# Kernel optimization log

Measured on AMD Instinct MI355X. Metric: run time of the kernel, lower is better.

## Reference

```python
import jax, jax.numpy as jnp
import numpy as np

N_NODE = 4096
K = 32           # num_nearest_neighbors
HIDDEN = 128
RMS_EPS = 1e-5
DT = 0.01        # init scale for linear weights (init_linear_weights(..., scale=dt))


def _rmsnorm(x, g):
    # RMSNorm over last dim with learned scale (eqx.nn.RMSNorm-style)
    return x * jax.lax.rsqrt(jnp.mean(x * x, axis=-1, keepdims=True) + RMS_EPS) * g


def _pos_mlp(x, W1, b1, g1, W2, b2, g2, W3, b3):
    # MLPWithLayerNorm(in=2, width=HIDDEN, depth=2, out=1, act=silu, rms_norm=True):
    # per hidden layer: Linear -> RMSNorm -> SiLU; final Linear with identity activation.
    h = jax.nn.silu(_rmsnorm(x @ W1.T + b1, g1))
    h = jax.nn.silu(_rmsnorm(h @ W2.T + b2, g2))
    return h @ W3.T + b3  # [E, 1]


def setup_inputs() -> dict:
    key = jax.random.key(0)
    ks = jax.random.split(key, 8)

    def xavier(k, shape):
        fan_in, fan_out = shape[1], shape[0]
        std = jnp.sqrt(2.0 / (fan_in + fan_out))
        return (jax.random.normal(k, shape, dtype=jnp.float32) * std * DT)

    return {
        "pos": jax.random.normal(ks[0], (N_NODE, 3), dtype=jnp.float32),
        "t": jax.random.uniform(ks[1], (1,), dtype=jnp.float32),
        "W1": xavier(ks[2], (HIDDEN, 2)),
        "b1": jnp.zeros((HIDDEN,), dtype=jnp.float32),
        "g1": jnp.ones((HIDDEN,), dtype=jnp.float32),
        "W2": xavier(ks[3], (HIDDEN, HIDDEN)),
        "b2": jnp.zeros((HIDDEN,), dtype=jnp.float32),
        "g2": jnp.ones((HIDDEN,), dtype=jnp.float32),
        "W3": xavier(ks[4], (1, HIDDEN)),
        "b3": jnp.zeros((1,), dtype=jnp.float32),
    }


def reference(pos, t, W1, b1, g1, W2, b2, g2, W3, b3):
    n = pos.shape[0]
    # Pairwise squared distances for kNN graph build
    diff = pos[:, None, :] - pos[None, :, :]              # [n, n, 3]
    radial_full = jnp.sum(diff * diff, axis=-1)           # [n, n]
    masked = radial_full.at[jnp.diag_indices(n)].set(jnp.inf)
    _, recv = jax.lax.top_k(-masked, k=K)                 # [n, K] nearest neighbors
    senders = jnp.repeat(jnp.arange(n), K)                # [n*K]
    receivers = recv.reshape(-1)                          # [n*K]

    # Gather edge geometry (normalize=False)
    coord_diff = pos[senders] - pos[receivers]            # [E, 3]
    radial = jnp.sum(coord_diff * coord_diff, axis=1, keepdims=True)  # [E, 1]

    # Per-edge MLP on [radial, t]
    t_scalar = jnp.reshape(t, ())
    edge_features = jnp.concatenate(
        [radial, jnp.full_like(radial, t_scalar)], axis=-1)          # [E, 2]
    edge_scalars = _pos_mlp(edge_features, W1, b1, g1, W2, b2, g2, W3, b3).squeeze(-1)

    # Scatter-sum messages back to sender nodes, average by neighbor count
    trans = coord_diff * edge_scalars[:, None]            # [E, 3]
    seg_sum = jax.ops.segment_sum(trans, senders, num_segments=n)    # [n, 3]
    seg_count = jnp.maximum(float(K), 1.0)
    return pos + seg_sum / seg_count
```

## Files before the change

### kernel.cpp

```cpp
#include <hip/hip_runtime.h>
#include <stdint.h>

#define NN   4096
#define KK   32
#define HID  128
#define BLK  256
#define WPB  4
#define GRID (NN / WPB)
#define CAP  128

typedef unsigned short bf16_t;
typedef __attribute__((ext_vector_type(8))) short bf16x8;
typedef __attribute__((ext_vector_type(4))) float f32x4;

#define FINF __uint_as_float(0x7f800000u)

__device__ __forceinline__ uint32_t pk2bf(float lo, float hi) {
    uint32_t r;
    asm("v_cvt_pk_bf16_f32 %0, %1, %2" : "=v"(r) : "v"(lo), "v"(hi));
    return r;
}
__device__ __forceinline__ float fastrcp(float x) {
    float r; asm("v_rcp_f32 %0, %1" : "=v"(r) : "v"(x)); return r;
}
__device__ __forceinline__ float fastrsq(float x) {
    float r; asm("v_rsq_f32 %0, %1" : "=v"(r) : "v"(x)); return r;
}
__device__ __forceinline__ float siluf(float x) {
    return x * fastrcp(1.0f + __expf(-x));
}

__device__ __forceinline__ void dist4(const float4* __restrict__ p4, int g, int lane,
                                      float px, float py, float pz,
                                      float d[4]) {
    float4 f0 = p4[g*192 + 3*lane];
    float4 f1 = p4[g*192 + 3*lane + 1];
    float4 f2 = p4[g*192 + 3*lane + 2];
    float jx[4] = {f0.x, f0.w, f1.z, f2.y};
    float jy[4] = {f0.y, f1.x, f1.w, f2.z};
    float jz[4] = {f0.z, f1.y, f2.x, f2.w};
    #pragma unroll
    for (int c = 0; c < 4; ++c) {
        float dx = px - jx[c], dy = py - jy[c], dz = pz - jz[c];
        d[c] = __fadd_rn(__fadd_rn(__fmul_rn(dx,dx), __fmul_rn(dy,dy)),
                         __fmul_rn(dz,dz));
    }
}

__global__ __launch_bounds__(256) void prepack_w2(
    const float* __restrict__ W2, uint4* __restrict__ w2b)
{
    int c  = blockIdx.x * 256 + threadIdx.x;
    int f  = c >> 6, ln = c & 63;
    int NT = f >> 2, kk = f & 3;
    int row = NT*16 + (ln & 15);
    int k0  = kk*32 + (ln >> 4) * 8;
    const float* s = W2 + row * HID + k0;
    float4 lo = *(const float4*)s;
    float4 hi = *(const float4*)(s + 4);
    uint4 pk;
    pk.x = pk2bf(lo.x, lo.y);
    pk.y = pk2bf(lo.z, lo.w);
    pk.z = pk2bf(hi.x, hi.y);
    pk.w = pk2bf(hi.z, hi.w);
    w2b[c] = pk;
}

template<bool WS>
struct __align__(16) Sm {
    union __align__(16) U {
        ushort dbf[NN];
        ushort h1[KK * HID];
    } uw[WPB];
    uint32_t cand[WPB][CAP];
    float    rads[WPB][KK];
    float    sedge[WPB][KK];
    int      recvs[WPB][KK];
    uint32_t w2l[WS ? 4 : HID * 64];
};

template<bool WS>
__global__ __launch_bounds__(BLK) void egnn_main(
    const float* __restrict__ pos, const float* __restrict__ tptr,
    const float* __restrict__ W1,  const float* __restrict__ b1,
    const float* __restrict__ g1,  const float* __restrict__ W2,
    const float* __restrict__ b2,  const float* __restrict__ g2,
    const float* __restrict__ W3,  const float* __restrict__ b3,
    const uint4* __restrict__ w2b, float* __restrict__ out)
{
    __shared__ Sm<WS> sm;
    const int tid  = threadIdx.x;
    const int lane = tid & 63;
    const int wid  = tid >> 6;
    const int i    = blockIdx.x * WPB + wid;
    const int l15  = lane & 15, lq = lane >> 4;

    const float ts  = tptr[0];
    const float b3s = b3[0];

    float A2, AC, C2;
    {
        const float4 w1v = ((const float4*)W1)[lane];
        const float2 b1v = ((const float2*)b1)[lane];
        float t0 = ts * w1v.y + b1v.x;
        float t1 = ts * w1v.w + b1v.y;
        A2 = w1v.x*w1v.x + w1v.z*w1v.z;
        AC = w1v.x*t0    + w1v.z*t1;
        C2 = t0*t0       + t1*t1;
        #pragma unroll
        for (int m = 32; m >= 1; m >>= 1) {
            A2 += __shfl_xor(A2, m, 64);
            AC += __shfl_xor(AC, m, 64);
            C2 += __shfl_xor(C2, m, 64);
        }
    }

    if constexpr (!WS) {
        for (int idx = tid; idx < HID * 16; idx += BLK) {
            int row = idx >> 4, c = idx & 15;
            const float* src = W2 + row * HID + c * 8;
            float4 lo = *(const float4*)src;
            float4 hi = *(const float4*)(src + 4);
            uint4 pk;
            pk.x = pk2bf(lo.x, lo.y);
            pk.y = pk2bf(lo.z, lo.w);
            pk.z = pk2bf(hi.x, hi.y);
            pk.w = pk2bf(hi.z, hi.w);
            *((uint4*)&sm.w2l[row * 64 + 4 * (c ^ (row & 15))]) = pk;
        }
        __syncthreads();
    }

    const float px = pos[3*i], py = pos[3*i+1], pz = pos[3*i+2];
    const float4* p4 = (const float4*)pos;

    const int  sgrp     = i >> 8;
    const bool selfLane = ((i >> 2) & 63) == lane;
    const int  selfc    = i & 3;

    float mind = FINF;
    {
        ushort* dbf = sm.uw[wid].dbf;
        #pragma unroll 4
        for (int g = 0; g < 16; ++g) {
            float d[4];
            dist4(p4, g, lane, px, py, pz, d);
            if (g == sgrp && selfLane) {
                #pragma unroll
                for (int c = 0; c < 4; ++c)
                    if (c == selfc) d[c] = FINF;
            }
            uint32_t lo = (__float_as_uint(d[0]) >> 16) | (__float_as_uint(d[1]) & 0xffff0000u);
            uint32_t hi = (__float_as_uint(d[2]) >> 16) | (__float_as_uint(d[3]) & 0xffff0000u);
            *((uint2*)&dbf[g*256 + 4*lane]) = make_uint2(lo, hi);
            mind = fminf(fminf(fminf(mind, d[0]), fminf(d[1], d[2])), d[3]);
        }
    }
    const uint32_t m16 = __float_as_uint(mind) >> 16;

    uint32_t v = 0;
    #pragma unroll
    for (int b = 15; b >= 0; --b) {
        uint32_t t = v | (1u << b);
        int nl = (int)__popcll(__ballot(m16 < t));
        if (nl < KK) v = t;
    }

    uint32_t cnt = 0;
    {
        const ushort* dbf = sm.uw[wid].dbf;
        uint32_t myc = 0;
        #pragma unroll 4
        for (int g = 0; g < 16; ++g) {
            uint2 w = *((const uint2*)&dbf[g*256 + 4*lane]);
            myc += (uint32_t)((w.x & 0xffffu) <= v);
            myc += (uint32_t)((w.x >> 16)     <= v);
            myc += (uint32_t)((w.y & 0xffffu) <= v);
            myc += (uint32_t)((w.y >> 16)     <= v);
        }
        uint32_t inc = myc;
        #pragma unroll
        for (int off = 1; off < 64; off <<= 1) {
            uint32_t y = __shfl_up(inc, off, 64);
            if (lane >= off) inc += y;
        }
        uint32_t slot = inc - myc;
        cnt = (uint32_t)__shfl((int)inc, 63, 64);
        if (myc) {
            #pragma unroll 4
            for (int g = 0; g < 16; ++g) {
                uint2 w = *((const uint2*)&dbf[g*256 + 4*lane]);
                uint32_t d16v[4] = {w.x & 0xffffu, w.x >> 16, w.y & 0xffffu, w.y >> 16};
                #pragma unroll
                for (int c = 0; c < 4; ++c) {
                    if (d16v[c] <= v) {
                        if (slot < CAP)
                            sm.cand[wid][slot] = (d16v[c] << 16)
                                               | (unsigned)(g*256 + 4*lane + c);
                        slot++;
                    }
                }
            }
        }
    }
    const int cntv = (int)cnt;

    if (cntv <= CAP) {
        for (int idx = cntv + lane; idx < CAP; idx += 64)
            sm.cand[wid][idx] = 0xffffffffu;

        #pragma unroll
        for (int h = 0; h < 2; ++h) {
            int idx = h*64 + lane;
            if (idx < cntv) {
                uint32_t km = sm.cand[wid][idx];
                int rank = 0;
                #pragma unroll 4
                for (int q = 0; q < CAP; q += 16) {
                    const uint4* cp = (const uint4*)&sm.cand[wid][q];
                    uint4 u0 = cp[0];
                    uint4 u1 = cp[1];
                    uint4 u2 = cp[2];
                    uint4 u3 = cp[3];
                    rank += (u0.x < km) ? 1 : 0;
                    rank += (u0.y < km) ? 1 : 0;
                    rank += (u0.z < km) ? 1 : 0;
                    rank += (u0.w < km) ? 1 : 0;
                    rank += (u1.x < km) ? 1 : 0;
                    rank += (u1.y < km) ? 1 : 0;
                    rank += (u1.z < km) ? 1 : 0;
                    rank += (u1.w < km) ? 1 : 0;
                    rank += (u2.x < km) ? 1 : 0;
                    rank += (u2.y < km) ? 1 : 0;
                    rank += (u2.z < km) ? 1 : 0;
                    rank += (u2.w < km) ? 1 : 0;
                    rank += (u3.x < km) ? 1 : 0;
                    rank += (u3.y < km) ? 1 : 0;
                    rank += (u3.z < km) ? 1 : 0;
                    rank += (u3.w < km) ? 1 : 0;
                }
                if (rank < KK) sm.recvs[wid][rank] = (int)(km & 0xFFFFu);
            }
        }
    } else {
        unsigned long long locmask = 0ull;
        if (selfLane)
            locmask |= 1ull << ((sgrp << 2) | selfc);
        for (int it = 0; it < KK; ++it) {
            unsigned long long best = ~0ull;
            for (int g = 0; g < 16; ++g) {
                float d[4];
                dist4(p4, g, lane, px, py, pz, d);
                #pragma unroll
                for (int c = 0; c < 4; ++c) {
                    bool dead = ((locmask >> (g*4 + c)) & 1ull) != 0ull;
                    unsigned long long key = dead ? ~0ull
                        : ((((unsigned long long)__float_as_uint(d[c])) << 12)
                           | (unsigned)(g*256 + 4*lane + c));
                    best = best < key ? best : key;
                }
            }
            #pragma unroll
            for (int m = 32; m >= 1; m >>= 1) {
                unsigned long long o = __shfl_xor(best, m, 64);
                best = best < o ? best : o;
            }
            int j = (int)(best & 0xfffull);
            if (lane == 0) sm.recvs[wid][it] = j;
            if (((j >> 2) & 63) == lane)
                locmask |= 1ull << ((j >> 8) * 4 + (j & 3));
        }
    }

    float cdx = 0.f, cdy = 0.f, cdz = 0.f;
    if (lane < KK) {
        int r = sm.recvs[wid][lane];
        cdx = px - pos[3*r];
        cdy = py - pos[3*r+1];
        cdz = pz - pos[3*r+2];
        float rad = __fadd_rn(__fadd_rn(__fmul_rn(cdx,cdx), __fmul_rn(cdy,cdy)),
                              __fmul_rn(cdz,cdz));
        sm.rads[wid][lane] = rad;
    }

    {
        const int ch = lane >> 2, epr = lane & 3;
        float4 wA = ((const float4*)W1)[ch*4    ];
        float4 wB = ((const float4*)W1)[ch*4 + 1];
        float4 wC = ((const float4*)W1)[ch*4 + 2];
        float4 wD = ((const float4*)W1)[ch*4 + 3];
        float4 bA = ((const float4*)b1)[ch*2], bB = ((const float4*)b1)[ch*2 + 1];
        float4 gA = ((const float4*)g1)[ch*2], gB = ((const float4*)g1)[ch*2 + 1];
        float av[8] = {wA.x, wA.z, wB.x, wB.z, wC.x, wC.z, wD.x, wD.z};
        float cv[8] = {ts*wA.y + bA.x, ts*wA.w + bA.y, ts*wB.y + bA.z, ts*wB.w + bA.w,
                       ts*wC.y + bB.x, ts*wC.w + bB.y, ts*wD.y + bB.z, ts*wD.w + bB.w};
        float gv[8] = {gA.x, gA.y, gA.z, gA.w, gB.x, gB.y, gB.z, gB.w};
        uint4* h1q = (uint4*)&sm.uw[wid].h1[0];
        #pragma unroll
        for (int g = 0; g < 8; ++g) {
            int E = 4*g + epr;
            float rad = sm.rads[wid][E];
            float sqv = rad*rad*A2 + 2.0f*rad*AC + C2;
            float rn  = fastrsq(sqv * (1.0f/HID) + 1e-5f);
            uint32_t pk[4];
            #pragma unroll
            for (int p = 0; p < 4; ++p) {
                float va = siluf((rad*av[2*p]   + cv[2*p])   * rn * gv[2*p]);
                float vb = siluf((rad*av[2*p+1] + cv[2*p+1]) * rn * gv[2*p+1]);
                pk[p] = pk2bf(va, vb);
            }
            h1q[E*16 + (ch ^ (E & 15))] = uint4{pk[0], pk[1], pk[2], pk[3]};
        }
    }

    float g2v[8], w3v[8], b2v[8];
    #pragma unroll
    for (int nt = 0; nt < 8; ++nt) {
        int n = nt*16 + l15;
        g2v[nt] = g2[n]; w3v[nt] = W3[n]; b2v[nt] = b2[n];
    }

    const bf16x8* h1v = (const bf16x8*)&sm.uw[wid].h1[0];
    #pragma unroll
    for (int mt = 0; mt < 2; ++mt) {
        f32x4 acc[8];
        #pragma unroll
        for (int nt = 0; nt < 8; ++nt) acc[nt] = f32x4{0.f, 0.f, 0.f, 0.f};
        const int m = mt*16 + l15;
        if constexpr (WS) {
            const bf16x8* bv = (const bf16x8*)w2b;
            #pragma unroll
            for (int kk = 0; kk < 4; ++kk) {
                bf16x8 af = h1v[m*16 + ((kk*4 + lq) ^ l15)];
                #pragma unroll
                for (int nt = 0; nt < 8; ++nt)
                    acc[nt] = __builtin_amdgcn_mfma_f32_16x16x32_bf16(
                                  af, bv[(nt*4 + kk)*64 + lane], acc[nt], 0, 0, 0);
            }
        } else {
            const bf16x8* w2v = (const bf16x8*)sm.w2l;
            #pragma unroll
            for (int kk = 0; kk < 4; ++kk) {
                const int q = (kk*4 + lq) ^ l15;
                bf16x8 af = h1v[m*16 + q];
                #pragma unroll
                for (int nt = 0; nt < 8; ++nt)
                    acc[nt] = __builtin_amdgcn_mfma_f32_16x16x32_bf16(
                                  af, w2v[(nt*16 + l15)*16 + q], acc[nt], 0, 0, 0);
            }
        }

        float ss[4];
        #pragma unroll
        for (int r = 0; r < 4; ++r) {
            float t = 0.f;
            #pragma unroll
            for (int nt = 0; nt < 8; ++nt) {
                float zz = acc[nt][r] + b2v[nt];
                acc[nt][r] = zz;
                t += zz*zz;
            }
            ss[r] = t;
        }
        #pragma unroll
        for (int m2 = 1; m2 <= 8; m2 <<= 1) {
            #pragma unroll
            for (int r = 0; r < 4; ++r) ss[r] += __shfl_xor(ss[r], m2, 64);
        }
        float sp[4];
        #pragma unroll
        for (int r = 0; r < 4; ++r) {
            float rn = fastrsq(ss[r] * (1.0f/HID) + 1e-5f);
            float t = 0.f;
            #pragma unroll
            for (int nt = 0; nt < 8; ++nt)
                t += siluf(acc[nt][r] * rn * g2v[nt]) * w3v[nt];
            sp[r] = t;
        }
        #pragma unroll
        for (int m2 = 1; m2 <= 8; m2 <<= 1) {
            #pragma unroll
            for (int r = 0; r < 4; ++r) sp[r] += __shfl_xor(sp[r], m2, 64);
        }
        if (l15 == 0) {
            #pragma unroll
            for (int r = 0; r < 4; ++r)
                sm.sedge[wid][mt*16 + lq*4 + r] = sp[r] + b3s;
        }
    }

    float mx = 0.f, my = 0.f, mz = 0.f;
    if (lane < KK) {
        float s = sm.sedge[wid][lane];
        mx = cdx * s; my = cdy * s; mz = cdz * s;
    }
    #pragma unroll
    for (int m = 32; m >= 1; m >>= 1) {
        mx += __shfl_xor(mx, m, 64);
        my += __shfl_xor(my, m, 64);
        mz += __shfl_xor(mz, m, 64);
    }
    if (lane == 0) {
        out[3*i    ] = px + mx * (1.0f/KK);
        out[3*i + 1] = py + my * (1.0f/KK);
        out[3*i + 2] = pz + mz * (1.0f/KK);
    }
}

extern "C" void kernel_launch(void* const* d_in, const int* in_sizes, int n_in,
                              void* d_out, int out_size, void* d_ws, size_t ws_size,
                              hipStream_t stream) {
    (void)in_sizes; (void)n_in; (void)out_size;
    const float* pos = (const float*)d_in[0];
    const float* t   = (const float*)d_in[1];
    const float* W1  = (const float*)d_in[2];
    const float* b1  = (const float*)d_in[3];
    const float* g1  = (const float*)d_in[4];
    const float* W2  = (const float*)d_in[5];
    const float* b2  = (const float*)d_in[6];
    const float* g2  = (const float*)d_in[7];
    const float* W3  = (const float*)d_in[8];
    const float* b3  = (const float*)d_in[9];
    float* out = (float*)d_out;

    if (d_ws != nullptr && ws_size >= 32768) {
        prepack_w2<<<8, 256, 0, stream>>>(W2, (uint4*)d_ws);
        egnn_main<true><<<GRID, BLK, 0, stream>>>(
            pos, t, W1, b1, g1, W2, b2, g2, W3, b3, (const uint4*)d_ws, out);
    } else {
        egnn_main<false><<<GRID, BLK, 0, stream>>>(
            pos, t, W1, b1, g1, W2, b2, g2, W3, b3, nullptr, out);
    }
}
```

Before: 109.3 us.

## Vectorize kNN distance math and register-buffer candidates to skip rescan

```diff
diff --git a/kernel.cpp b/kernel.cpp
--- a/kernel.cpp
+++ b/kernel.cpp
@@ -12,6 +12,7 @@
 typedef unsigned short bf16_t;
 typedef __attribute__((ext_vector_type(8))) short bf16x8;
 typedef __attribute__((ext_vector_type(4))) float f32x4;
+typedef __attribute__((ext_vector_type(2))) float f32x2;
 
 #define FINF __uint_as_float(0x7f800000u)
 
@@ -30,21 +31,29 @@
     return x * fastrcp(1.0f + __expf(-x));
 }
 
-__device__ __forceinline__ void dist4(const float4* __restrict__ p4, int g, int lane,
-                                      float px, float py, float pz,
-                                      float d[4]) {
+__device__ __forceinline__ void dist4v(const float4* __restrict__ p4, int g, int lane,
+                                       f32x2 pxv, f32x2 pyv, f32x2 pzv,
+                                       f32x2& d01, f32x2& d23) {
     float4 f0 = p4[g*192 + 3*lane];
     float4 f1 = p4[g*192 + 3*lane + 1];
     float4 f2 = p4[g*192 + 3*lane + 2];
-    float jx[4] = {f0.x, f0.w, f1.z, f2.y};
-    float jy[4] = {f0.y, f1.x, f1.w, f2.z};
-    float jz[4] = {f0.z, f1.y, f2.x, f2.w};
-    #pragma unroll
-    for (int c = 0; c < 4; ++c) {
-        float dx = px - jx[c], dy = py - jy[c], dz = pz - jz[c];
-        d[c] = __fadd_rn(__fadd_rn(__fmul_rn(dx,dx), __fmul_rn(dy,dy)),
-                         __fmul_rn(dz,dz));
-    }
+    f32x2 jx0 = {f0.x, f0.w}, jx1 = {f1.z, f2.y};
+    f32x2 jy0 = {f0.y, f1.x}, jy1 = {f1.w, f2.z};
+    f32x2 jz0 = {f0.z, f1.y}, jz1 = {f2.x, f2.w};
+    {
+#pragma clang fp contract(off)
+        f32x2 dx0 = pxv - jx0, dy0 = pyv - jy0, dz0 = pzv - jz0;
+        f32x2 dx1 = pxv - jx1, dy1 = pyv - jy1, dz1 = pzv - jz1;
+        d01 = dx0*dx0 + dy0*dy0 + dz0*dz0;
+        d23 = dx1*dx1 + dy1*dy1 + dz1*dz1;
+    }
+}
+__device__ __forceinline__ void dist4s(const float4* __restrict__ p4, int g, int lane,
+                                       float px, float py, float pz, float d[4]) {
+    f32x2 pxv = {px, px}, pyv = {py, py}, pzv = {pz, pz};
+    f32x2 a, b;
+    dist4v(p4, g, lane, pxv, pyv, pzv, a, b);
+    d[0] = a.x; d[1] = a.y; d[2] = b.x; d[3] = b.y;
 }
 
 __global__ __launch_bounds__(256) void prepack_w2(
@@ -133,6 +142,7 @@
 
     const float px = pos[3*i], py = pos[3*i+1], pz = pos[3*i+2];
     const float4* p4 = (const float4*)pos;
+    const f32x2 pxv = {px, px}, pyv = {py, py}, pzv = {pz, pz};
 
     const int  sgrp     = i >> 8;
     const bool selfLane = ((i >> 2) & 63) == lane;
@@ -143,17 +153,21 @@
         ushort* dbf = sm.uw[wid].dbf;
         #pragma unroll 4
         for (int g = 0; g < 16; ++g) {
-            float d[4];
-            dist4(p4, g, lane, px, py, pz, d);
+            f32x2 d01, d23;
+            dist4v(p4, g, lane, pxv, pyv, pzv, d01, d23);
             if (g == sgrp && selfLane) {
-                #pragma unroll
-                for (int c = 0; c < 4; ++c)
-                    if (c == selfc) d[c] = FINF;
-            }
-            uint32_t lo = (__float_as_uint(d[0]) >> 16) | (__float_as_uint(d[1]) & 0xffff0000u);
-            uint32_t hi = (__float_as_uint(d[2]) >> 16) | (__float_as_uint(d[3]) & 0xffff0000u);
+                d01.x = (selfc == 0) ? FINF : d01.x;
+                d01.y = (selfc == 1) ? FINF : d01.y;
+                d23.x = (selfc == 2) ? FINF : d23.x;
+                d23.y = (selfc == 3) ? FINF : d23.y;
+            }
+            uint2 u0 = *(uint2*)&d01;
+            uint2 u1 = *(uint2*)&d23;
+            uint32_t lo = (u0.x >> 16) | (u0.y & 0xffff0000u);
+            uint32_t hi = (u1.x >> 16) | (u1.y & 0xffff0000u);
             *((uint2*)&dbf[g*256 + 4*lane]) = make_uint2(lo, hi);
-            mind = fminf(fminf(fminf(mind, d[0]), fminf(d[1], d[2])), d[3]);
+            f32x2 mm = __builtin_elementwise_min(d01, d23);
+            mind = fminf(mind, fminf(mm.x, mm.y));
         }
     }
     const uint32_t m16 = __float_as_uint(mind) >> 16;
@@ -167,26 +181,46 @@
     }
 
     uint32_t cnt = 0;
+    uint32_t myc = 0;
     {
         const ushort* dbf = sm.uw[wid].dbf;
-        uint32_t myc = 0;
+        uint32_t s0 = 0, s1 = 0, s2 = 0, s3 = 0, s4 = 0, s5 = 0;
         #pragma unroll 4
         for (int g = 0; g < 16; ++g) {
             uint2 w = *((const uint2*)&dbf[g*256 + 4*lane]);
-            myc += (uint32_t)((w.x & 0xffffu) <= v);
-            myc += (uint32_t)((w.x >> 16)     <= v);
-            myc += (uint32_t)((w.y & 0xffffu) <= v);
-            myc += (uint32_t)((w.y >> 16)     <= v);
+            uint32_t e[4] = {w.x & 0xffffu, w.x >> 16, w.y & 0xffffu, w.y >> 16};
+            #pragma unroll
+            for (int c = 0; c < 4; ++c) {
+                if (e[c] <= v) {
+                    uint32_t key = (e[c] << 16) | (unsigned)(g*256 + 4*lane + c);
+                    s0 = (myc == 0) ? key : s0;
+                    s1 = (myc == 1) ? key : s1;
+                    s2 = (myc == 2) ? key : s2;
+                    s3 = (myc == 3) ? key : s3;
+                    s4 = (myc == 4) ? key : s4;
+                    s5 = (myc == 5) ? key : s5;
+                    myc++;
+                }
+            }
         }
         uint32_t inc = myc;
         #pragma unroll
         for (int off = 1; off < 64; off <<= 1) {
-            uint32_t y = __shfl_up(inc, off, 64);
+            uint32_t y = (uint32_t)__shfl_up((int)inc, off, 64);
             if (lane >= off) inc += y;
         }
         uint32_t slot = inc - myc;
         cnt = (uint32_t)__shfl((int)inc, 63, 64);
-        if (myc) {
+
+        const bool ovf = __ballot(myc > 6) != 0ull;
+        if (!ovf) {
+            if (myc > 0 && slot     < CAP) sm.cand[wid][slot    ] = s0;
+            if (myc > 1 && slot + 1 < CAP) sm.cand[wid][slot + 1] = s1;
+            if (myc > 2 && slot + 2 < CAP) sm.cand[wid][slot + 2] = s2;
+            if (myc > 3 && slot + 3 < CAP) sm.cand[wid][slot + 3] = s3;
+            if (myc > 4 && slot + 4 < CAP) sm.cand[wid][slot + 4] = s4;
+            if (myc > 5 && slot + 5 < CAP) sm.cand[wid][slot + 5] = s5;
+        } else if (myc) {
             #pragma unroll 4
             for (int g = 0; g < 16; ++g) {
                 uint2 w = *((const uint2*)&dbf[g*256 + 4*lane]);
@@ -209,15 +243,15 @@
         for (int idx = cntv + lane; idx < CAP; idx += 64)
             sm.cand[wid][idx] = 0xffffffffu;
 
+        const int nb = (cntv + 15) >> 4;
         #pragma unroll
         for (int h = 0; h < 2; ++h) {
             int idx = h*64 + lane;
             if (idx < cntv) {
                 uint32_t km = sm.cand[wid][idx];
                 int rank = 0;
-                #pragma unroll 4
-                for (int q = 0; q < CAP; q += 16) {
-                    const uint4* cp = (const uint4*)&sm.cand[wid][q];
+                for (int q = 0; q < nb; ++q) {
+                    const uint4* cp = (const uint4*)&sm.cand[wid][q*16];
                     uint4 u0 = cp[0];
                     uint4 u1 = cp[1];
                     uint4 u2 = cp[2];
@@ -250,7 +284,7 @@
             unsigned long long best = ~0ull;
             for (int g = 0; g < 16; ++g) {
                 float d[4];
-                dist4(p4, g, lane, px, py, pz, d);
+                dist4s(p4, g, lane, px, py, pz, d);
                 #pragma unroll
                 for (int c = 0; c < 4; ++c) {
                     bool dead = ((locmask >> (g*4 + c)) & 1ull) != 0ull;
```

New measurement: 108.0 us. No clear change (-1.2%).

## Pack distance math, use LDS atomics for candidate compaction, bound rank loop

Applied to the files above, without the earlier changes.

```diff
diff --git a/kernel.cpp b/kernel.cpp
--- a/kernel.cpp
+++ b/kernel.cpp
@@ -12,6 +12,7 @@
 typedef unsigned short bf16_t;
 typedef __attribute__((ext_vector_type(8))) short bf16x8;
 typedef __attribute__((ext_vector_type(4))) float f32x4;
+typedef __attribute__((ext_vector_type(2))) float f32x2;
 
 #define FINF __uint_as_float(0x7f800000u)
 
@@ -29,10 +30,15 @@
 __device__ __forceinline__ float siluf(float x) {
     return x * fastrcp(1.0f + __expf(-x));
 }
-
-__device__ __forceinline__ void dist4(const float4* __restrict__ p4, int g, int lane,
-                                      float px, float py, float pz,
-                                      float d[4]) {
+__device__ __forceinline__ f32x2 pk_add(f32x2 a, f32x2 b) {
+    f32x2 r; asm("v_pk_add_f32 %0, %1, %2" : "=v"(r) : "v"(a), "v"(b)); return r;
+}
+__device__ __forceinline__ f32x2 pk_sq(f32x2 a) {
+    f32x2 r; asm("v_pk_mul_f32 %0, %1, %1" : "=v"(r) : "v"(a)); return r;
+}
+
+__device__ __forceinline__ void dist4s(const float4* __restrict__ p4, int g, int lane,
+                                       float px, float py, float pz, float d[4]) {
     float4 f0 = p4[g*192 + 3*lane];
     float4 f1 = p4[g*192 + 3*lane + 1];
     float4 f2 = p4[g*192 + 3*lane + 2];
@@ -73,6 +79,7 @@
         ushort h1[KK * HID];
     } uw[WPB];
     uint32_t cand[WPB][CAP];
+    uint32_t ccnt[WPB];
     float    rads[WPB][KK];
     float    sedge[WPB][KK];
     int      recvs[WPB][KK];
@@ -95,6 +102,8 @@
     const int i    = blockIdx.x * WPB + wid;
     const int l15  = lane & 15, lq = lane >> 4;
 
+    if (lane == 0) sm.ccnt[wid] = 0;
+
     const float ts  = tptr[0];
     const float b3s = b3[0];
 
@@ -133,6 +142,7 @@
 
     const float px = pos[3*i], py = pos[3*i+1], pz = pos[3*i+2];
     const float4* p4 = (const float4*)pos;
+    const f32x2 nPxy = {-px, -py}, nPzx = {-pz, -px}, nPyz = {-py, -pz};
 
     const int  sgrp     = i >> 8;
     const bool selfLane = ((i >> 2) & 63) == lane;
@@ -143,17 +153,31 @@
         ushort* dbf = sm.uw[wid].dbf;
         #pragma unroll 4
         for (int g = 0; g < 16; ++g) {
-            float d[4];
-            dist4(p4, g, lane, px, py, pz, d);
+            float4 f0 = p4[g*192 + 3*lane];
+            float4 f1 = p4[g*192 + 3*lane+1];
+            float4 f2 = p4[g*192 + 3*lane+2];
+            f32x2 S0 = pk_sq(pk_add(f32x2{f0.x, f0.y}, nPxy));
+            f32x2 S1 = pk_sq(pk_add(f32x2{f0.z, f0.w}, nPzx));
+            f32x2 S2 = pk_sq(pk_add(f32x2{f1.x, f1.y}, nPyz));
+            f32x2 S3 = pk_sq(pk_add(f32x2{f1.z, f1.w}, nPxy));
+            f32x2 S4 = pk_sq(pk_add(f32x2{f2.x, f2.y}, nPzx));
+            f32x2 S5 = pk_sq(pk_add(f32x2{f2.z, f2.w}, nPyz));
+            float d0 = S0.x + S0.y + S1.x;
+            float d1 = S1.y + S2.x + S2.y;
+            float d2 = S3.x + S3.y + S4.x;
+            float d3 = S4.y + S5.x + S5.y;
             if (g == sgrp && selfLane) {
-                #pragma unroll
-                for (int c = 0; c < 4; ++c)
-                    if (c == selfc) d[c] = FINF;
-            }
-            uint32_t lo = (__float_as_uint(d[0]) >> 16) | (__float_as_uint(d[1]) & 0xffff0000u);
-            uint32_t hi = (__float_as_uint(d[2]) >> 16) | (__float_as_uint(d[3]) & 0xffff0000u);
+                d0 = (selfc == 0) ? FINF : d0;
+                d1 = (selfc == 1) ? FINF : d1;
+                d2 = (selfc == 2) ? FINF : d2;
+                d3 = (selfc == 3) ? FINF : d3;
+            }
+            uint32_t lo = __builtin_amdgcn_perm(__float_as_uint(d1),
+                                                __float_as_uint(d0), 0x07060302u);
+            uint32_t hi = __builtin_amdgcn_perm(__float_as_uint(d3),
+                                                __float_as_uint(d2), 0x07060302u);
             *((uint2*)&dbf[g*256 + 4*lane]) = make_uint2(lo, hi);
-            mind = fminf(fminf(fminf(mind, d[0]), fminf(d[1], d[2])), d[3]);
+            mind = fminf(fminf(fminf(mind, d0), fminf(d1, d2)), d3);
         }
     }
     const uint32_t m16 = __float_as_uint(mind) >> 16;
@@ -166,42 +190,29 @@
         if (nl < KK) v = t;
     }
 
-    uint32_t cnt = 0;
+    uint32_t cnt;
     {
         const ushort* dbf = sm.uw[wid].dbf;
-        uint32_t myc = 0;
+        const uint32_t vk  = (v << 16) | 0xffffu;
+        const uint32_t jb0 = 4*lane;
         #pragma unroll 4
         for (int g = 0; g < 16; ++g) {
             uint2 w = *((const uint2*)&dbf[g*256 + 4*lane]);
-            myc += (uint32_t)((w.x & 0xffffu) <= v);
-            myc += (uint32_t)((w.x >> 16)     <= v);
-            myc += (uint32_t)((w.y & 0xffffu) <= v);
-            myc += (uint32_t)((w.y >> 16)     <= v);
-        }
-        uint32_t inc = myc;
-        #pragma unroll
-        for (int off = 1; off < 64; off <<= 1) {
-            uint32_t y = __shfl_up(inc, off, 64);
-            if (lane >= off) inc += y;
-        }
-        uint32_t slot = inc - myc;
-        cnt = (uint32_t)__shfl((int)inc, 63, 64);
-        if (myc) {
-            #pragma unroll 4
-            for (int g = 0; g < 16; ++g) {
-                uint2 w = *((const uint2*)&dbf[g*256 + 4*lane]);
-                uint32_t d16v[4] = {w.x & 0xffffu, w.x >> 16, w.y & 0xffffu, w.y >> 16};
-                #pragma unroll
-                for (int c = 0; c < 4; ++c) {
-                    if (d16v[c] <= v) {
-                        if (slot < CAP)
-                            sm.cand[wid][slot] = (d16v[c] << 16)
-                                               | (unsigned)(g*256 + 4*lane + c);
-                        slot++;
-                    }
-                }
-            }
-        }
+            uint32_t jb = jb0 + g*256;
+            uint32_t k0 = (w.x << 16) | jb;
+            uint32_t k1 = (w.x & 0xffff0000u) | (jb + 1);
+            uint32_t k2 = (w.y << 16) | (jb + 2);
+            uint32_t k3 = (w.y & 0xffff0000u) | (jb + 3);
+            if (k0 <= vk) { uint32_t s = atomicAdd(&sm.ccnt[wid], 1u);
+                            if (s < CAP) sm.cand[wid][s] = k0; }
+            if (k1 <= vk) { uint32_t s = atomicAdd(&sm.ccnt[wid], 1u);
+                            if (s < CAP) sm.cand[wid][s] = k1; }
+            if (k2 <= vk) { uint32_t s = atomicAdd(&sm.ccnt[wid], 1u);
+                            if (s < CAP) sm.cand[wid][s] = k2; }
+            if (k3 <= vk) { uint32_t s = atomicAdd(&sm.ccnt[wid], 1u);
+                            if (s < CAP) sm.cand[wid][s] = k3; }
+        }
+        cnt = sm.ccnt[wid];
     }
     const int cntv = (int)cnt;
 
@@ -209,15 +220,15 @@
         for (int idx = cntv + lane; idx < CAP; idx += 64)
             sm.cand[wid][idx] = 0xffffffffu;
 
+        const int nb = (cntv + 15) >> 4;
         #pragma unroll
         for (int h = 0; h < 2; ++h) {
             int idx = h*64 + lane;
             if (idx < cntv) {
                 uint32_t km = sm.cand[wid][idx];
                 int rank = 0;
-                #pragma unroll 4
-                for (int q = 0; q < CAP; q += 16) {
-                    const uint4* cp = (const uint4*)&sm.cand[wid][q];
+                for (int q = 0; q < nb; ++q) {
+                    const uint4* cp = (const uint4*)&sm.cand[wid][q*16];
                     uint4 u0 = cp[0];
                     uint4 u1 = cp[1];
                     uint4 u2 = cp[2];
@@ -250,7 +261,7 @@
             unsigned long long best = ~0ull;
             for (int g = 0; g < 16; ++g) {
                 float d[4];
-                dist4(p4, g, lane, px, py, pz, d);
+                dist4s(p4, g, lane, px, py, pz, d);
                 #pragma unroll
                 for (int c = 0; c < 4; ++c) {
                     bool dead = ((locmask >> (g*4 + c)) & 1ull) != 0ull;
```

Result: no change. 107.8 us (-1.3%).
